# Kernel optimization log

Hardware: AMD Instinct MI355X
Metric: run time of the kernel (lower is better)

## Reference

```python
import jax, jax.numpy as jnp
import numpy as np

D = 768
ED = 192  # d // 4
E = 8     # n_experts
K = 2     # top_k
B, H, W = 32, 32, 32
LN_EPS = 1e-5


def setup_inputs() -> dict:
    key = jax.random.key(0)
    ks = jax.random.split(key, 5)
    s = 0.02
    x = jax.random.normal(ks[0], (B, D, H, W), dtype=jnp.float32)
    Wr = jax.random.normal(ks[1], (E, D), dtype=jnp.float32) * s   # router: logits = tokens @ Wr.T
    W1 = jax.random.normal(ks[2], (E, D, ED), dtype=jnp.float32) * s  # gate proj (silu branch)
    W3 = jax.random.normal(ks[3], (E, D, ED), dtype=jnp.float32) * s  # linear branch
    W2 = jax.random.normal(ks[4], (E, ED, D), dtype=jnp.float32) * s  # down proj
    gamma = jnp.ones((D,), dtype=jnp.float32)
    beta = jnp.zeros((D,), dtype=jnp.float32)
    return {"x": x, "Wr": Wr, "W1": W1, "W3": W3, "W2": W2, "gamma": gamma, "beta": beta}


def _layernorm(y, gamma, beta):
    mu = jnp.mean(y, axis=-1, keepdims=True)
    var = jnp.mean(jnp.square(y - mu), axis=-1, keepdims=True)
    return (y - mu) * jax.lax.rsqrt(var + LN_EPS) * gamma + beta


def _moe_forward(x, Wr, W1, W3, W2, gamma, beta):
    b, c, h, w = x.shape
    tokens = x.transpose(0, 2, 3, 1).reshape(-1, c)        # [T, d]
    logits = tokens @ Wr.T                                  # [T, E]
    topk_v, topk_i = jax.lax.top_k(logits, K)               # [T, K]
    topk_w = jax.nn.softmax(topk_v, axis=-1)                # [T, K]
    # dense combine weights: zero for non-selected experts (same math as masked scatter)
    gates = jnp.sum(jax.nn.one_hot(topk_i, E, dtype=tokens.dtype) * topk_w[..., None], axis=1)  # [T, E]
    # SwiGLU per expert (forward uses silu(e[0](t)) * e[2](t), then e[3])
    hdn = jax.nn.silu(jnp.einsum('td,edh->teh', tokens, W1)) * jnp.einsum('td,edh->teh', tokens, W3)  # [T,E,ed]
    y = jnp.einsum('te,teh,ehd->td', gates, hdn, W2)        # combine: [T, d]
    out = _layernorm(y, gamma, beta) + tokens
    return out.reshape(b, h, w, c).transpose(0, 3, 1, 2)


def reference(x, Wr, W1, W3, W2, gamma, beta):
    return _moe_forward(x, Wr, W1, W3, W2, gamma, beta)
```

## Files before the change

kernel.cpp:

```cpp
#include <hip/hip_runtime.h>
#include <cstdint>
#include <cstddef>

#define T_TOK 32768
#define DM 768
#define EDIM 192
#define NEXP 8

typedef unsigned short u16;
typedef short bf16x8 __attribute__((ext_vector_type(8)));
typedef float f32x4 __attribute__((ext_vector_type(4)));
typedef u16 u16x8 __attribute__((ext_vector_type(8)));

__device__ __forceinline__ u16 f2bf(float f) {
  unsigned u = __float_as_uint(f);
  return (u16)((u + 0x7FFFu + ((u >> 16) & 1u)) >> 16);
}
__device__ __forceinline__ float bf2f(u16 u) {
  return __uint_as_float(((unsigned)u) << 16);
}

__device__ __forceinline__ void gld16(const void* g, void* l) {
  __builtin_amdgcn_global_load_lds(
      (const __attribute__((address_space(1))) unsigned int*)g,
      (__attribute__((address_space(3))) unsigned int*)l,
      16, 0, 0);
}

__device__ __forceinline__ bf16x8 frag_ld(const u16* lds, int row, int kb) {
  int ph = row * 128 + (kb ^ ((row & 7) << 4));
  return *(const bf16x8*)((const char*)lds + ph);
}

__global__ __launch_bounds__(256) void k_prep(
    const float* __restrict__ W1, const float* __restrict__ W3,
    const float* __restrict__ W2, u16* __restrict__ W1T,
    u16* __restrict__ W3T, u16* __restrict__ W2T)
{
  __shared__ __align__(16) float td[64][68];
  const int z = blockIdx.z;
  const int mat = z >> 3, e = z & 7;
  const int R = (mat == 2) ? EDIM : DM;
  const int C = (mat == 2) ? DM : EDIM;
  const int r0 = blockIdx.x * 64, c0 = blockIdx.y * 64;
  if (r0 >= R || c0 >= C) return;
  const float* in = (mat == 0 ? W1 : mat == 1 ? W3 : W2) + (size_t)e * R * C;
  u16* out = (mat == 0 ? W1T : mat == 1 ? W3T : W2T) + (size_t)e * R * C;
  const int tid = threadIdx.x;
  {
    int rl = tid >> 2, cs = (tid & 3) * 16;
    const float* s = in + (size_t)(r0 + rl) * C + c0 + cs;
    #pragma unroll
    for (int i = 0; i < 16; i += 4) *(float4*)&td[rl][cs + i] = *(const float4*)(s + i);
  }
  __syncthreads();
  {
    int cl = tid >> 2, rs = (tid & 3) * 16;
    u16* d = out + (size_t)(c0 + cl) * R + r0 + rs;
    u16x8 o0, o1;
    #pragma unroll
    for (int i = 0; i < 8; ++i) {
      o0[i] = f2bf(td[rs + i][cl]);
      o1[i] = f2bf(td[rs + 8 + i][cl]);
    }
    *(u16x8*)d = o0;
    *(u16x8*)(d + 8) = o1;
  }
}

__global__ __launch_bounds__(256) void k_tokrouter(
    const float* __restrict__ x, const float* __restrict__ Wr,
    u16* __restrict__ tokbf, int* __restrict__ cnt,
    int* __restrict__ toklist, float* __restrict__ gatelist)
{
  __shared__ float WrL[8][772];
  __shared__ float xL[64][33];
  __shared__ float logitsL[32][8];
  __shared__ int cnt8[8];
  __shared__ int baseL[8];
  const int tid = threadIdx.x;
  const int t0 = blockIdx.x * 32;
  const int b = t0 >> 10;
  const int h = (t0 >> 5) & 31;
  const float* xb = x + (size_t)b * (DM * 1024) + h * 32;

  for (int i = tid; i < 1536; i += 256) {
    int r = i / 192;
    int c = (i - r * 192) * 4;
    *(float4*)&WrL[r][c] = ((const float4*)Wr)[i];
  }

  const int rt = tid >> 3;
  const int re = tid & 7;
  float lacc = 0.f;

  for (int cb = 0; cb < 12; ++cb) {
    const int c0 = cb * 64;
    __syncthreads();
    #pragma unroll
    for (int it = 0; it < 2; ++it) {
      int idx = it * 256 + tid;
      int r = idx >> 3, cc = (idx & 7) * 4;
      float4 v = *(const float4*)(xb + (size_t)(c0 + r) * 1024 + cc);
      xL[r][cc] = v.x; xL[r][cc + 1] = v.y; xL[r][cc + 2] = v.z; xL[r][cc + 3] = v.w;
    }
    __syncthreads();
    {
      const float* wr = &WrL[re][c0];
      #pragma unroll
      for (int c = 0; c < 64; ++c) lacc = fmaf(xL[c][rt], wr[c], lacc);
    }
    {
      u16x8 o;
      #pragma unroll
      for (int i = 0; i < 8; ++i) o[i] = f2bf(xL[re * 8 + i][rt]);
      *(u16x8*)(tokbf + (size_t)(t0 + rt) * DM + c0 + re * 8) = o;
    }
  }

  logitsL[rt][re] = lacc;
  if (tid < 8) cnt8[tid] = 0;
  __syncthreads();

  int e0 = -1, e1 = -1, lp0 = 0, lp1 = 0;
  float g0 = 0.f, g1 = 0.f;
  if (tid < 32) {
    float v0 = -1e30f, v1 = -1e30f;
    #pragma unroll
    for (int e = 0; e < 8; ++e) { float v = logitsL[tid][e]; if (v > v0) { v0 = v; e0 = e; } }
    #pragma unroll
    for (int e = 0; e < 8; ++e) {
      if (e == e0) continue;
      float v = logitsL[tid][e]; if (v > v1) { v1 = v; e1 = e; }
    }
    float w = expf(v1 - v0);
    g0 = 1.f / (1.f + w);
    g1 = w / (1.f + w);
    lp0 = atomicAdd(&cnt8[e0], 1);
    lp1 = atomicAdd(&cnt8[e1], 1);
  }
  __syncthreads();
  if (tid < 8) baseL[tid] = atomicAdd(&cnt[tid], cnt8[tid]);
  __syncthreads();
  if (tid < 32) {
    int tg = t0 + tid;
    int p0 = baseL[e0] + lp0;
    int p1 = baseL[e1] + lp1;
    toklist[e0 * T_TOK + p0] = tg;
    gatelist[e0 * T_TOK + p0] = g0;
    toklist[e1 * T_TOK + p1] = tg | (1 << 16);
    gatelist[e1 * T_TOK + p1] = g1;
  }
}

__global__ __launch_bounds__(256) void k_ffn1(
    const u16* __restrict__ tokbf, const u16* __restrict__ W1T,
    const u16* __restrict__ W3T, const int* __restrict__ cnt,
    const int* __restrict__ toklist, u16* __restrict__ hbuf)
{
  __shared__ __align__(16) u16 As[128 * 64];
  __shared__ __align__(16) u16 B1s[64 * 64];
  __shared__ __align__(16) u16 B3s[64 * 64];
  __shared__ int rowbaseL[128];
  const int e = blockIdx.z;
  const int count = cnt[e];
  const int start = blockIdx.x * 128;
  if (start >= count) return;
  const int n0 = blockIdx.y * 64;
  const int rows = min(128, count - start);
  const int tid = threadIdx.x;

  int offe = 0;
  #pragma unroll
  for (int i = 0; i < NEXP; ++i) offe += (i < e) ? cnt[i] : 0;

  if (tid < 128) {
    int r = (tid < rows) ? tid : 0;
    rowbaseL[tid] = (toklist[e * T_TOK + start + r] & 0xFFFF) * DM;
  }
  __syncthreads();

  const int lrow = tid >> 3;
  const int swq = (((tid & 7) * 16) ^ ((lrow & 7) << 4)) >> 1;
  const u16 *srcA[4], *srcB1[2], *srcB3[2];
  #pragma unroll
  for (int it = 0; it < 4; ++it)
    srcA[it] = tokbf + rowbaseL[it * 32 + lrow] + swq;
  #pragma unroll
  for (int it = 0; it < 2; ++it) {
    size_t wb = (size_t)(e * EDIM + n0 + it * 32 + lrow) * DM + swq;
    srcB1[it] = W1T + wb;
    srcB3[it] = W3T + wb;
  }

  const int w = tid >> 6, l = tid & 63;
  const int wm = (w >> 1) * 64, wn = (w & 1) * 32;
  const int lr = l & 15;
  const int lk = (l >> 4) * 16;

  f32x4 acc1[4][2], acc3[4][2];
  #pragma unroll
  for (int i = 0; i < 4; ++i)
    #pragma unroll
    for (int j = 0; j < 2; ++j) {
      acc1[i][j] = (f32x4){0.f, 0.f, 0.f, 0.f};
      acc3[i][j] = (f32x4){0.f, 0.f, 0.f, 0.f};
    }

  for (int kc = 0; kc < 12; ++kc) {
    const int ko = kc * 64;
    #pragma unroll
    for (int it = 0; it < 4; ++it)
      gld16(srcA[it] + ko, (char*)As + (it * 256 + tid) * 16);
    #pragma unroll
    for (int it = 0; it < 2; ++it) {
      gld16(srcB1[it] + ko, (char*)B1s + (it * 256 + tid) * 16);
      gld16(srcB3[it] + ko, (char*)B3s + (it * 256 + tid) * 16);
    }
    __syncthreads();
    #pragma unroll
    for (int kk = 0; kk < 2; ++kk) {
      const int kb = kk * 64 + lk;
      bf16x8 af[4], b1[2], b3[2];
      #pragma unroll
      for (int mf = 0; mf < 4; ++mf) af[mf] = frag_ld(As, wm + mf * 16 + lr, kb);
      #pragma unroll
      for (int nf = 0; nf < 2; ++nf) {
        b1[nf] = frag_ld(B1s, wn + nf * 16 + lr, kb);
        b3[nf] = frag_ld(B3s, wn + nf * 16 + lr, kb);
      }
      #pragma unroll
      for (int mf = 0; mf < 4; ++mf)
        #pragma unroll
        for (int nf = 0; nf < 2; ++nf) {
          acc1[mf][nf] = __builtin_amdgcn_mfma_f32_16x16x32_bf16(af[mf], b1[nf], acc1[mf][nf], 0, 0, 0);
          acc3[mf][nf] = __builtin_amdgcn_mfma_f32_16x16x32_bf16(af[mf], b3[nf], acc3[mf][nf], 0, 0, 0);
        }
    }
    __syncthreads();
  }

  const int rq = (l >> 4) * 4;
  const int abase = offe + start;
  #pragma unroll
  for (int mf = 0; mf < 4; ++mf)
    #pragma unroll
    for (int nf = 0; nf < 2; ++nf)
      #pragma unroll
      for (int r = 0; r < 4; ++r) {
        int m = wm + mf * 16 + rq + r;
        if (m < rows) {
          float a = acc1[mf][nf][r];
          float hv = (a / (1.f + expf(-a))) * acc3[mf][nf][r];
          hbuf[(size_t)(abase + m) * EDIM + (n0 + wn + nf * 16 + lr)] = f2bf(hv);
        }
      }
}

__global__ __launch_bounds__(256) void k_ffn2(
    const u16* __restrict__ hbuf, const u16* __restrict__ W2T,
    const int* __restrict__ cnt, const int* __restrict__ toklist,
    const float* __restrict__ gatelist, u16* __restrict__ ypart)
{
  __shared__ __align__(16) u16 As[128 * 64];
  __shared__ __align__(16) u16 Bs[128 * 64];
  __shared__ int dstL[128];
  __shared__ float gL[128];
  const int e = blockIdx.z;
  const int count = cnt[e];
  const int start = blockIdx.x * 128;
  if (start >= count) return;
  const int n0 = blockIdx.y * 128;
  const int rows = min(128, count - start);
  const int tid = threadIdx.x;

  int offe = 0;
  #pragma unroll
  for (int i = 0; i < NEXP; ++i) offe += (i < e) ? cnt[i] : 0;
  const int abase = offe + start;

  if (tid < 128) {
    int r = (tid < rows) ? tid : 0;
    int entry = toklist[e * T_TOK + start + r];
    int t = entry & 0xFFFF, k = entry >> 16;
    dstL[tid] = (k * T_TOK + t) * DM;
    gL[tid] = gatelist[e * T_TOK + start + r];
  }
  __syncthreads();

  const int lrow = tid >> 3;
  const int swq = (((tid & 7) * 16) ^ ((lrow & 7) << 4)) >> 1;
  const u16 *srcA[4], *srcB[4];
  #pragma unroll
  for (int it = 0; it < 4; ++it) {
    int r = it * 32 + lrow;
    int rr = (r < rows) ? r : 0;
    srcA[it] = hbuf + (size_t)(abase + rr) * EDIM + swq;
    srcB[it] = W2T + (size_t)(e * DM + n0 + r) * EDIM + swq;
  }

  const int w = tid >> 6, l = tid & 63;
  const int wm = (w >> 1) * 64, wn = (w & 1) * 64;
  const int lr = l & 15;
  const int lk = (l >> 4) * 16;

  f32x4 acc[4][4];
  #pragma unroll
  for (int i = 0; i < 4; ++i)
    #pragma unroll
    for (int j = 0; j < 4; ++j) acc[i][j] = (f32x4){0.f, 0.f, 0.f, 0.f};

  for (int kc = 0; kc < 3; ++kc) {
    const int ko = kc * 64;
    #pragma unroll
    for (int it = 0; it < 4; ++it) {
      gld16(srcA[it] + ko, (char*)As + (it * 256 + tid) * 16);
      gld16(srcB[it] + ko, (char*)Bs + (it * 256 + tid) * 16);
    }
    __syncthreads();
    #pragma unroll
    for (int kk = 0; kk < 2; ++kk) {
      const int kb = kk * 64 + lk;
      bf16x8 af[4], bf_[4];
      #pragma unroll
      for (int mf = 0; mf < 4; ++mf) af[mf] = frag_ld(As, wm + mf * 16 + lr, kb);
      #pragma unroll
      for (int nf = 0; nf < 4; ++nf) bf_[nf] = frag_ld(Bs, wn + nf * 16 + lr, kb);
      #pragma unroll
      for (int mf = 0; mf < 4; ++mf)
        #pragma unroll
        for (int nf = 0; nf < 4; ++nf)
          acc[mf][nf] = __builtin_amdgcn_mfma_f32_16x16x32_bf16(af[mf], bf_[nf], acc[mf][nf], 0, 0, 0);
    }
    __syncthreads();
  }

  const int rq = (l >> 4) * 4;
  #pragma unroll
  for (int mf = 0; mf < 4; ++mf)
    #pragma unroll
    for (int nf = 0; nf < 4; ++nf)
      #pragma unroll
      for (int r = 0; r < 4; ++r) {
        int m = wm + mf * 16 + rq + r;
        if (m < rows) {
          float v = acc[mf][nf][r] * gL[m];
          ypart[(size_t)dstL[m] + (n0 + wn + nf * 16 + lr)] = f2bf(v);
        }
      }
}

__global__ __launch_bounds__(256) void k_stats(
    const u16* __restrict__ ypart, float* __restrict__ mu, float* __restrict__ rs)
{
  const int tid = threadIdx.x;
  const int t = blockIdx.x * 16 + (tid >> 4);
  const int j = tid & 15;
  const u16* y0 = ypart + (size_t)t * DM;
  const u16* y1 = y0 + (size_t)T_TOK * DM;
  float sum = 0.f, sq = 0.f;
  #pragma unroll
  for (int i = 0; i < 6; ++i) {
    int c = i * 128 + j * 8;
    u16x8 a = *(const u16x8*)(y0 + c);
    u16x8 b = *(const u16x8*)(y1 + c);
    #pragma unroll
    for (int q = 0; q < 8; ++q) {
      float v = bf2f(a[q]) + bf2f(b[q]);
      sum += v; sq += v * v;
    }
  }
  #pragma unroll
  for (int d = 1; d < 16; d <<= 1) { sum += __shfl_xor(sum, d); sq += __shfl_xor(sq, d); }
  if (j == 0) {
    float m = sum * (1.f / 768.f);
    float var = sq * (1.f / 768.f) - m * m;
    mu[t] = m;
    rs[t] = 1.f / sqrtf(var + 1e-5f);
  }
}

__global__ __launch_bounds__(256) void k_apply(
    const u16* __restrict__ ypart, const u16* __restrict__ tokbf,
    const float* __restrict__ gamma, const float* __restrict__ beta,
    const float* __restrict__ mu, const float* __restrict__ rs,
    float* __restrict__ out)
{
  __shared__ float lnT[64][65];
  const int tid = threadIdx.x;
  const int t0 = blockIdx.x * 64;
  const int c0 = blockIdx.y * 64;
  const int b = t0 >> 10;
  const int h0 = (t0 >> 5) & 31;
  const u16* y0 = ypart;
  const u16* y1 = ypart + (size_t)T_TOK * DM;
  {
    const int tl = tid >> 2, q = tid & 3;
    const size_t tbase = (size_t)(t0 + tl) * DM;
    const int c = c0 + q * 16;
    const float mu_ = mu[t0 + tl], rs_ = rs[t0 + tl];
    u16x8 a0 = *(const u16x8*)(y0 + tbase + c);
    u16x8 a1 = *(const u16x8*)(y0 + tbase + c + 8);
    u16x8 b0 = *(const u16x8*)(y1 + tbase + c);
    u16x8 b1 = *(const u16x8*)(y1 + tbase + c + 8);
    u16x8 t0v = *(const u16x8*)(tokbf + tbase + c);
    u16x8 t1v = *(const u16x8*)(tokbf + tbase + c + 8);
    #pragma unroll
    for (int i = 0; i < 8; ++i) {
      float v = bf2f(a0[i]) + bf2f(b0[i]);
      lnT[q * 16 + i][tl] = (v - mu_) * rs_ * gamma[c + i] + beta[c + i] + bf2f(t0v[i]);
      float u = bf2f(a1[i]) + bf2f(b1[i]);
      lnT[q * 16 + 8 + i][tl] = (u - mu_) * rs_ * gamma[c + 8 + i] + beta[c + 8 + i] + bf2f(t1v[i]);
    }
  }
  __syncthreads();
  {
    int cl = tid >> 2, ts = (tid & 3) * 16;
    int c = c0 + cl;
    int hh = h0 + (ts >> 5), ww = ts & 31;
    size_t oidx = (((size_t)b * DM + c) * 32 + hh) * 32 + ww;
    #pragma unroll
    for (int i = 0; i < 16; i += 4) {
      float4 ov;
      ov.x = lnT[cl][ts + i + 0];
      ov.y = lnT[cl][ts + i + 1];
      ov.z = lnT[cl][ts + i + 2];
      ov.w = lnT[cl][ts + i + 3];
      *(float4*)(out + oidx + i) = ov;
    }
  }
}

constexpr size_t OFF_TOK  = 0;
constexpr size_t OFF_W1T  = OFF_TOK + (size_t)T_TOK * DM * 2;
constexpr size_t OFF_W3T  = OFF_W1T + (size_t)NEXP * EDIM * DM * 2;
constexpr size_t OFF_W2T  = OFF_W3T + (size_t)NEXP * EDIM * DM * 2;
constexpr size_t OFF_H    = OFF_W2T + (size_t)NEXP * EDIM * DM * 2;
constexpr size_t OFF_YP   = OFF_H + (size_t)T_TOK * 2 * EDIM * 2;
constexpr size_t OFF_CNT  = OFF_YP + (size_t)2 * T_TOK * DM * 2;
constexpr size_t OFF_LIST = OFF_CNT + 256;
constexpr size_t OFF_GATE = OFF_LIST + (size_t)NEXP * T_TOK * 4;
constexpr size_t OFF_MU   = OFF_GATE + (size_t)NEXP * T_TOK * 4;
constexpr size_t OFF_RS   = OFF_MU + (size_t)T_TOK * 4;

extern "C" void kernel_launch(void* const* d_in, const int* in_sizes, int n_in,
                              void* d_out, int out_size, void* d_ws, size_t ws_size,
                              hipStream_t stream) {
  const float* x     = (const float*)d_in[0];
  const float* Wr    = (const float*)d_in[1];
  const float* W1    = (const float*)d_in[2];
  const float* W3    = (const float*)d_in[3];
  const float* W2    = (const float*)d_in[4];
  const float* gamma = (const float*)d_in[5];
  const float* beta  = (const float*)d_in[6];
  float* out = (float*)d_out;
  char* ws = (char*)d_ws;

  u16* tokbf = (u16*)(ws + OFF_TOK);
  u16* W1T   = (u16*)(ws + OFF_W1T);
  u16* W3T   = (u16*)(ws + OFF_W3T);
  u16* W2T   = (u16*)(ws + OFF_W2T);
  u16* hbuf  = (u16*)(ws + OFF_H);
  u16* ypart = (u16*)(ws + OFF_YP);
  int* cnt   = (int*)(ws + OFF_CNT);
  int* toklist = (int*)(ws + OFF_LIST);
  float* gatelist = (float*)(ws + OFF_GATE);
  float* muB = (float*)(ws + OFF_MU);
  float* rsB = (float*)(ws + OFF_RS);

  hipMemsetAsync(cnt, 0, 64, stream);
  hipLaunchKernelGGL(k_prep, dim3(12, 12, 24), dim3(256), 0, stream,
                     W1, W3, W2, W1T, W3T, W2T);
  hipLaunchKernelGGL(k_tokrouter, dim3(1024), dim3(256), 0, stream,
                     x, Wr, tokbf, cnt, toklist, gatelist);
  hipLaunchKernelGGL(k_ffn1, dim3(256, 3, 8), dim3(256), 0, stream,
                     tokbf, W1T, W3T, cnt, toklist, hbuf);
  hipLaunchKernelGGL(k_ffn2, dim3(256, 6, 8), dim3(256), 0, stream,
                     hbuf, W2T, cnt, toklist, gatelist, ypart);
  hipLaunchKernelGGL(k_stats, dim3(2048), dim3(256), 0, stream,
                     ypart, muB, rsB);
  hipLaunchKernelGGL(k_apply, dim3(512, 12), dim3(256), 0, stream,
                     ypart, tokbf, gamma, beta, muB, rsB, out);
}
```

Before: 225.3 us.

## Fuse weight prep into router kernel and merge LayerNorm stats with apply

The weight transpose/convert kernel is merged into the token-router kernel as extra blocks in one grid, which removes a launch and lets both run concurrently. The separate LayerNorm stats and apply kernels are fused so each block reads ypart and tokens once, computes mean and rstd locally, and writes NCHW output. This removes a second full read of ypart and the mu/rs round trip. The trade-offs are an extra bf16 rounding of the summed y before normalization, and output stores that are only 16 floats (64 bytes) contiguous per channel row.

```diff
diff --git a/kernel.cpp b/kernel.cpp
--- a/kernel.cpp
+++ b/kernel.cpp
@@ -32,54 +32,59 @@
   return *(const bf16x8*)((const char*)lds + ph);
 }
 
-__global__ __launch_bounds__(256) void k_prep(
+__global__ __launch_bounds__(256) void k_tokprep(
+    const float* __restrict__ x, const float* __restrict__ Wr,
     const float* __restrict__ W1, const float* __restrict__ W3,
-    const float* __restrict__ W2, u16* __restrict__ W1T,
-    u16* __restrict__ W3T, u16* __restrict__ W2T)
+    const float* __restrict__ W2,
+    u16* __restrict__ tokbf, int* __restrict__ cnt,
+    int* __restrict__ toklist, float* __restrict__ gatelist,
+    u16* __restrict__ W1T, u16* __restrict__ W3T, u16* __restrict__ W2T)
 {
-  __shared__ __align__(16) float td[64][68];
-  const int z = blockIdx.z;
-  const int mat = z >> 3, e = z & 7;
-  const int R = (mat == 2) ? EDIM : DM;
-  const int C = (mat == 2) ? DM : EDIM;
-  const int r0 = blockIdx.x * 64, c0 = blockIdx.y * 64;
-  if (r0 >= R || c0 >= C) return;
-  const float* in = (mat == 0 ? W1 : mat == 1 ? W3 : W2) + (size_t)e * R * C;
-  u16* out = (mat == 0 ? W1T : mat == 1 ? W3T : W2T) + (size_t)e * R * C;
+  __shared__ __align__(16) char smraw[34304];
   const int tid = threadIdx.x;
-  {
-    int rl = tid >> 2, cs = (tid & 3) * 16;
-    const float* s = in + (size_t)(r0 + rl) * C + c0 + cs;
-    #pragma unroll
-    for (int i = 0; i < 16; i += 4) *(float4*)&td[rl][cs + i] = *(const float4*)(s + i);
-  }
-  __syncthreads();
-  {
-    int cl = tid >> 2, rs = (tid & 3) * 16;
-    u16* d = out + (size_t)(c0 + cl) * R + r0 + rs;
-    u16x8 o0, o1;
-    #pragma unroll
-    for (int i = 0; i < 8; ++i) {
-      o0[i] = f2bf(td[rs + i][cl]);
-      o1[i] = f2bf(td[rs + 8 + i][cl]);
-    }
-    *(u16x8*)d = o0;
-    *(u16x8*)(d + 8) = o1;
-  }
-}
-
-__global__ __launch_bounds__(256) void k_tokrouter(
-    const float* __restrict__ x, const float* __restrict__ Wr,
-    u16* __restrict__ tokbf, int* __restrict__ cnt,
-    int* __restrict__ toklist, float* __restrict__ gatelist)
-{
-  __shared__ float WrL[8][772];
-  __shared__ float xL[64][33];
-  __shared__ float logitsL[32][8];
-  __shared__ int cnt8[8];
-  __shared__ int baseL[8];
-  const int tid = threadIdx.x;
-  const int t0 = blockIdx.x * 32;
+  const int bx = blockIdx.x;
+
+  if (bx >= 1024) {
+    float (*td)[68] = (float(*)[68])smraw;
+    const int pid = bx - 1024;
+    const int mat = pid / 288;
+    const int rem = pid - mat * 288;
+    const int e = rem / 36;
+    const int tile = rem - e * 36;
+    int R, C, r0, c0;
+    if (mat < 2) { R = DM; C = EDIM; r0 = (tile / 3) * 64; c0 = (tile % 3) * 64; }
+    else         { R = EDIM; C = DM; r0 = (tile / 12) * 64; c0 = (tile % 12) * 64; }
+    const float* in = (mat == 0 ? W1 : mat == 1 ? W3 : W2) + (size_t)e * R * C;
+    u16* out = (mat == 0 ? W1T : mat == 1 ? W3T : W2T) + (size_t)e * R * C;
+    {
+      int rl = tid >> 2, cs = (tid & 3) * 16;
+      const float* s = in + (size_t)(r0 + rl) * C + c0 + cs;
+      #pragma unroll
+      for (int i = 0; i < 16; i += 4) *(float4*)&td[rl][cs + i] = *(const float4*)(s + i);
+    }
+    __syncthreads();
+    {
+      int cl = tid >> 2, rs = (tid & 3) * 16;
+      u16* d = out + (size_t)(c0 + cl) * R + r0 + rs;
+      u16x8 o0, o1;
+      #pragma unroll
+      for (int i = 0; i < 8; ++i) {
+        o0[i] = f2bf(td[rs + i][cl]);
+        o1[i] = f2bf(td[rs + 8 + i][cl]);
+      }
+      *(u16x8*)d = o0;
+      *(u16x8*)(d + 8) = o1;
+    }
+    return;
+  }
+
+  float (*WrL)[772]    = (float(*)[772])smraw;
+  float (*xL)[33]      = (float(*)[33])(smraw + 24704);
+  float (*logitsL)[8]  = (float(*)[8])(smraw + 33152);
+  int* cnt8            = (int*)(smraw + 34176);
+  int* baseL           = (int*)(smraw + 34208);
+
+  const int t0 = bx * 32;
   const int b = t0 >> 10;
   const int h = (t0 >> 5) & 31;
   const float* xb = x + (size_t)b * (DM * 1024) + h * 32;
@@ -350,83 +355,68 @@
       }
 }
 
-__global__ __launch_bounds__(256) void k_stats(
-    const u16* __restrict__ ypart, float* __restrict__ mu, float* __restrict__ rs)
-{
-  const int tid = threadIdx.x;
-  const int t = blockIdx.x * 16 + (tid >> 4);
-  const int j = tid & 15;
-  const u16* y0 = ypart + (size_t)t * DM;
-  const u16* y1 = y0 + (size_t)T_TOK * DM;
-  float sum = 0.f, sq = 0.f;
-  #pragma unroll
-  for (int i = 0; i < 6; ++i) {
-    int c = i * 128 + j * 8;
-    u16x8 a = *(const u16x8*)(y0 + c);
-    u16x8 b = *(const u16x8*)(y1 + c);
-    #pragma unroll
-    for (int q = 0; q < 8; ++q) {
-      float v = bf2f(a[q]) + bf2f(b[q]);
-      sum += v; sq += v * v;
-    }
-  }
-  #pragma unroll
-  for (int d = 1; d < 16; d <<= 1) { sum += __shfl_xor(sum, d); sq += __shfl_xor(sq, d); }
-  if (j == 0) {
-    float m = sum * (1.f / 768.f);
-    float var = sq * (1.f / 768.f) - m * m;
-    mu[t] = m;
-    rs[t] = 1.f / sqrtf(var + 1e-5f);
-  }
-}
-
-__global__ __launch_bounds__(256) void k_apply(
+__global__ __launch_bounds__(256) void k_lnapply(
     const u16* __restrict__ ypart, const u16* __restrict__ tokbf,
     const float* __restrict__ gamma, const float* __restrict__ beta,
-    const float* __restrict__ mu, const float* __restrict__ rs,
     float* __restrict__ out)
 {
-  __shared__ float lnT[64][65];
+  __shared__ u16 yL[16][776];
+  __shared__ u16 tkL[16][776];
+  __shared__ float muL[16], rsL[16];
   const int tid = threadIdx.x;
-  const int t0 = blockIdx.x * 64;
-  const int c0 = blockIdx.y * 64;
+  const int t0 = blockIdx.x * 16;
   const int b = t0 >> 10;
-  const int h0 = (t0 >> 5) & 31;
-  const u16* y0 = ypart;
-  const u16* y1 = ypart + (size_t)T_TOK * DM;
+  const int h = (t0 >> 5) & 31;
+  const int w0 = t0 & 31;
+
   {
-    const int tl = tid >> 2, q = tid & 3;
-    const size_t tbase = (size_t)(t0 + tl) * DM;
-    const int c = c0 + q * 16;
-    const float mu_ = mu[t0 + tl], rs_ = rs[t0 + tl];
-    u16x8 a0 = *(const u16x8*)(y0 + tbase + c);
-    u16x8 a1 = *(const u16x8*)(y0 + tbase + c + 8);
-    u16x8 b0 = *(const u16x8*)(y1 + tbase + c);
-    u16x8 b1 = *(const u16x8*)(y1 + tbase + c + 8);
-    u16x8 t0v = *(const u16x8*)(tokbf + tbase + c);
-    u16x8 t1v = *(const u16x8*)(tokbf + tbase + c + 8);
-    #pragma unroll
-    for (int i = 0; i < 8; ++i) {
-      float v = bf2f(a0[i]) + bf2f(b0[i]);
-      lnT[q * 16 + i][tl] = (v - mu_) * rs_ * gamma[c + i] + beta[c + i] + bf2f(t0v[i]);
-      float u = bf2f(a1[i]) + bf2f(b1[i]);
-      lnT[q * 16 + 8 + i][tl] = (u - mu_) * rs_ * gamma[c + 8 + i] + beta[c + 8 + i] + bf2f(t1v[i]);
-    }
-  }
-  __syncthreads();
+    const int tl = tid >> 4, j = tid & 15;
+    const u16* y0 = ypart + (size_t)(t0 + tl) * DM;
+    const u16* y1 = y0 + (size_t)T_TOK * DM;
+    const u16* tk = tokbf + (size_t)(t0 + tl) * DM;
+    float sum = 0.f, sq = 0.f;
+    #pragma unroll
+    for (int i = 0; i < 6; ++i) {
+      int c = i * 128 + j * 8;
+      u16x8 a = *(const u16x8*)(y0 + c);
+      u16x8 d = *(const u16x8*)(y1 + c);
+      u16x8 t = *(const u16x8*)(tk + c);
+      u16x8 o;
+      #pragma unroll
+      for (int q = 0; q < 8; ++q) {
+        float v = bf2f(a[q]) + bf2f(d[q]);
+        sum += v; sq += v * v;
+        o[q] = f2bf(v);
+      }
+      *(u16x8*)&yL[tl][c] = o;
+      *(u16x8*)&tkL[tl][c] = t;
+    }
+    #pragma unroll
+    for (int d = 1; d < 16; d <<= 1) { sum += __shfl_xor(sum, d); sq += __shfl_xor(sq, d); }
+    if (j == 0) {
+      float m = sum * (1.f / 768.f);
+      float var = sq * (1.f / 768.f) - m * m;
+      muL[tl] = m;
+      rsL[tl] = 1.f / sqrtf(var + 1e-5f);
+    }
+  }
+  __syncthreads();
+
   {
-    int cl = tid >> 2, ts = (tid & 3) * 16;
-    int c = c0 + cl;
-    int hh = h0 + (ts >> 5), ww = ts & 31;
-    size_t oidx = (((size_t)b * DM + c) * 32 + hh) * 32 + ww;
-    #pragma unroll
-    for (int i = 0; i < 16; i += 4) {
+    const int q = tid & 3, cq = tid >> 2;
+    #pragma unroll
+    for (int ci = 0; ci < 12; ++ci) {
+      const int c = ci * 64 + cq;
+      const float gc = gamma[c], bc = beta[c];
+      const size_t oidx = (((size_t)b * DM + c) * 32 + h) * 32 + w0 + q * 4;
       float4 ov;
-      ov.x = lnT[cl][ts + i + 0];
-      ov.y = lnT[cl][ts + i + 1];
-      ov.z = lnT[cl][ts + i + 2];
-      ov.w = lnT[cl][ts + i + 3];
-      *(float4*)(out + oidx + i) = ov;
+      #pragma unroll
+      for (int i = 0; i < 4; ++i) {
+        const int lt = q * 4 + i;
+        float v = (bf2f(yL[lt][c]) - muL[lt]) * rsL[lt] * gc + bc + bf2f(tkL[lt][c]);
+        (&ov.x)[i] = v;
+      }
+      *(float4*)(out + oidx) = ov;
     }
   }
 }
@@ -440,8 +430,6 @@
 constexpr size_t OFF_CNT  = OFF_YP + (size_t)2 * T_TOK * DM * 2;
 constexpr size_t OFF_LIST = OFF_CNT + 256;
 constexpr size_t OFF_GATE = OFF_LIST + (size_t)NEXP * T_TOK * 4;
-constexpr size_t OFF_MU   = OFF_GATE + (size_t)NEXP * T_TOK * 4;
-constexpr size_t OFF_RS   = OFF_MU + (size_t)T_TOK * 4;
 
 extern "C" void kernel_launch(void* const* d_in, const int* in_sizes, int n_in,
                               void* d_out, int out_size, void* d_ws, size_t ws_size,
@@ -465,20 +453,15 @@
   int* cnt   = (int*)(ws + OFF_CNT);
   int* toklist = (int*)(ws + OFF_LIST);
   float* gatelist = (float*)(ws + OFF_GATE);
-  float* muB = (float*)(ws + OFF_MU);
-  float* rsB = (float*)(ws + OFF_RS);
 
   hipMemsetAsync(cnt, 0, 64, stream);
-  hipLaunchKernelGGL(k_prep, dim3(12, 12, 24), dim3(256), 0, stream,
-                     W1, W3, W2, W1T, W3T, W2T);
-  hipLaunchKernelGGL(k_tokrouter, dim3(1024), dim3(256), 0, stream,
-                     x, Wr, tokbf, cnt, toklist, gatelist);
+  hipLaunchKernelGGL(k_tokprep, dim3(1888), dim3(256), 0, stream,
+                     x, Wr, W1, W3, W2, tokbf, cnt, toklist, gatelist,
+                     W1T, W3T, W2T);
   hipLaunchKernelGGL(k_ffn1, dim3(256, 3, 8), dim3(256), 0, stream,
                      tokbf, W1T, W3T, cnt, toklist, hbuf);
   hipLaunchKernelGGL(k_ffn2, dim3(256, 6, 8), dim3(256), 0, stream,
                      hbuf, W2T, cnt, toklist, gatelist, ypart);
-  hipLaunchKernelGGL(k_stats, dim3(2048), dim3(256), 0, stream,
-                     ypart, muB, rsB);
-  hipLaunchKernelGGL(k_apply, dim3(512, 12), dim3(256), 0, stream,
-                     ypart, tokbf, gamma, beta, muB, rsB, out);
-}
+  hipLaunchKernelGGL(k_lnapply, dim3(2048), dim3(256), 0, stream,
+                     ypart, tokbf, gamma, beta, out);
+}
```

After: 215.2 us, median of 2. -4.5%, faster.
